# Kernel tuning notes

Hardware: AMD Instinct MI355X
Metric: run time of the kernel (lower is better)

## Reference

```python
import jax, jax.numpy as jnp
import numpy as np

F = 32  # node channels (both convs)


def ecc_conv(x, src, dst, e, fgn_w, fgn_b, root, bias):
    """Edge-conditioned conv: per-edge kernel from edge feats, gather-matmul-scatter."""
    n_nodes = x.shape[0]
    n_edges = e.shape[0]
    f_in = x.shape[1]
    # filter-generating network: (E, S) -> (E, F_in*F_out) -> (E, F_in, F_out)
    kernels = (e @ fgn_w + fgn_b).reshape(n_edges, f_in, F)
    # gather source node feats, per-edge matmul
    messages = jnp.einsum('ef,efo->eo', x[src], kernels)
    # scatter-sum to target nodes
    agg = jax.ops.segment_sum(messages, dst, num_segments=n_nodes)
    return jax.nn.relu(agg + x @ root + bias)


def setup_inputs() -> dict:
    key = jax.random.key(0)
    ks = jax.random.split(key, 12)
    N, E, S = 50000, 200000, 16
    s = 0.05  # small init scale to keep activations bounded through relu
    return {
        'x': jax.random.normal(ks[0], (N, F), jnp.float32),
        'e': jax.random.normal(ks[1], (E, S), jnp.float32),
        'src': jax.random.randint(ks[2], (E,), 0, N, jnp.int32),
        'dst': jax.random.randint(ks[3], (E,), 0, N, jnp.int32),
        'fgn_w1': jax.random.normal(ks[4], (S, F * F), jnp.float32) * s,
        'fgn_b1': jnp.zeros((F * F,), jnp.float32),
        'root1': jax.random.normal(ks[5], (F, F), jnp.float32) * s,
        'bias1': jnp.zeros((F,), jnp.float32),
        'fgn_w2': jax.random.normal(ks[6], (S, F * F), jnp.float32) * s,
        'fgn_b2': jnp.zeros((F * F,), jnp.float32),
        'root2': jax.random.normal(ks[7], (F, F), jnp.float32) * s,
        'bias2': jnp.zeros((F,), jnp.float32),
        'dense_w': jax.random.normal(ks[8], (F, 1), jnp.float32) * s,
        'dense_b': jnp.zeros((1,), jnp.float32),
    }


def reference(x, e, src, dst, fgn_w1, fgn_b1, root1, bias1,
              fgn_w2, fgn_b2, root2, bias2, dense_w, dense_b):
    h = ecc_conv(x, src, dst, e, fgn_w1, fgn_b1, root1, bias1)
    h = ecc_conv(h, src, dst, e, fgn_w2, fgn_b2, root2, bias2)
    pooled = jnp.sum(h, axis=0)          # global sum pool over nodes -> (F,)
    return pooled @ dense_w + dense_b    # (1,)
```

## Files before the change

kernel.cpp:

```cpp
#include <hip/hip_runtime.h>
#include <hip/hip_bf16.h>

#define F 32
#define S 16

typedef short v8s __attribute__((ext_vector_type(8)));
typedef float v4f __attribute__((ext_vector_type(4)));

__device__ __forceinline__ float bf_lo(unsigned u) { return __uint_as_float(u << 16); }
__device__ __forceinline__ float bf_hi(unsigned u) { return __uint_as_float(u & 0xffff0000u); }
__device__ __forceinline__ unsigned short f2bf(float f) {
    __hip_bfloat16 h = __float2bfloat16(f);
    return *(unsigned short*)&h;
}
__device__ __forceinline__ unsigned pack2(float a, float b) {
    __hip_bfloat162 h2 = __float22bfloat162_rn(make_float2(a, b));
    return *(unsigned*)&h2;
}
static inline size_t align256(size_t b) { return (b + 255) & ~(size_t)255; }

__global__ __launch_bounds__(256) void convert_w2(
    const float* __restrict__ w1, const float* __restrict__ b1, const float* __restrict__ r1,
    const float* __restrict__ w2, const float* __restrict__ b2, const float* __restrict__ r2,
    unsigned short* __restrict__ Wf1, unsigned short* __restrict__ Wf2,
    unsigned short* __restrict__ Rt1, unsigned short* __restrict__ Rt2)
{
    const int PER = 34 * 512 + 32 * 32;
    int tid = blockIdx.x * blockDim.x + threadIdx.x;
    if (tid >= 2 * PER) return;
    const int layer = tid / PER;
    const int rem   = tid % PER;
    const float* w = layer ? w2 : w1;
    const float* b = layer ? b2 : b1;
    const float* r = layer ? r2 : r1;
    if (rem < 34 * 512) {
        const int fi   = rem >> 9;
        const int rr   = rem & 511;
        const int lane = rr >> 3;
        const int j    = rr & 7;
        const int half = fi & 1;
        const int ck   = fi >> 1;
        const int o    = (half << 4) | (lane & 15);
        const int k    = ck * 32 + (lane >> 4) * 8 + j;
        const int s    = k >> 5, f = k & 31;
        const float v  = (s < S) ? w[s * (F * F) + f * F + o] : b[f * F + o];
        (layer ? Wf2 : Wf1)[rem] = f2bf(v);
    } else {
        const int q = rem - 34 * 512;
        const int o = q >> 5, f = q & 31;
        (layer ? Rt2 : Rt1)[o * F + f] = f2bf(r[f * F + o]);
    }
}

__global__ __launch_bounds__(256) void hist_kernel(
    const int* __restrict__ dst, int* __restrict__ cnt, int E)
{
    int e = blockIdx.x * blockDim.x + threadIdx.x;
    if (e < E) atomicAdd(&cnt[dst[e]], 1);
}

__global__ __launch_bounds__(256) void scan_partial(
    const int* __restrict__ cnt, int* __restrict__ partial, int N)
{
    const int i = blockIdx.x * 256 + threadIdx.x;
    int v = (i < N) ? cnt[i] : 0;
    #pragma unroll
    for (int off = 32; off > 0; off >>= 1) v += __shfl_down(v, off, 64);
    __shared__ int wsum[4];
    const int wave = threadIdx.x >> 6, lane = threadIdx.x & 63;
    if (lane == 0) wsum[wave] = v;
    __syncthreads();
    if (threadIdx.x == 0)
        partial[blockIdx.x] = wsum[0] + wsum[1] + wsum[2] + wsum[3];
}

__global__ void scan_top(int* __restrict__ partial, int M)
{
    const int t = threadIdx.x;
    int carry = 0;
    for (int base = 0; base < M; base += 64) {
        const int i = base + t;
        const int v0 = (i < M) ? partial[i] : 0;
        int v = v0;
        #pragma unroll
        for (int off = 1; off < 64; off <<= 1) {
            int u = __shfl_up(v, off, 64);
            if (t >= off) v += u;
        }
        if (i < M) partial[i] = carry + (v - v0);
        carry += __shfl(v, 63, 64);
    }
}

__global__ __launch_bounds__(256) void scan_final(
    const int* __restrict__ cnt, const int* __restrict__ partial,
    int* __restrict__ cursor, int* __restrict__ rowptr, int N)
{
    const int i = blockIdx.x * 256 + threadIdx.x;
    const int v0 = (i < N) ? cnt[i] : 0;
    int v = v0;
    const int wave = threadIdx.x >> 6, lane = threadIdx.x & 63;
    #pragma unroll
    for (int off = 1; off < 64; off <<= 1) {
        int u = __shfl_up(v, off, 64);
        if (lane >= off) v += u;
    }
    __shared__ int wsum[4];
    if (lane == 63) wsum[wave] = v;
    __syncthreads();
    int woff = 0;
    for (int ww = 0; ww < 4; ++ww) woff += (ww < wave) ? wsum[ww] : 0;
    if (i < N) {
        const int excl = partial[blockIdx.x] + woff + (v - v0);
        cursor[i] = excl;
        rowptr[i] = excl;
    }
}

__global__ __launch_bounds__(256) void scatter_kernel(
    const int* __restrict__ dst, int* __restrict__ cursor,
    int* __restrict__ perm, int E)
{
    int e = blockIdx.x * blockDim.x + threadIdx.x;
    if (e < E) {
        int p = atomicAdd(&cursor[dst[e]], 1);
        perm[p] = e;
    }
}

__global__ __launch_bounds__(256) void esort_kernel(
    const float* __restrict__ ef, const int* __restrict__ src,
    const int* __restrict__ perm,
    float* __restrict__ ef_s, int* __restrict__ src_s, int E)
{
    const int gid = blockIdx.x * blockDim.x + threadIdx.x;
    const int slot = gid >> 2;
    if (slot >= E) return;
    const int q = gid & 3;
    const int e = perm[slot];
    ((float4*)(ef_s + (size_t)slot * S))[q] = ((const float4*)(ef + (size_t)e * S))[q];
    if (q == 0) src_s[slot] = src[e];
}

__global__ __launch_bounds__(256) void edge_msg(
    const float* __restrict__ xin,
    const float* __restrict__ ef_s,
    const int* __restrict__ src_s,
    const unsigned short* __restrict__ Wf,
    unsigned short* __restrict__ msg,
    int E)
{
    __shared__ v8s Wl[34 * 64];
    const int tid  = threadIdx.x;
    const int w    = tid >> 6;
    const int lane = tid & 63;
    const int lid  = lane & 15;
    const int quad = lane >> 4;

    {
        const uint4* s = (const uint4*)Wf;
        uint4* d = (uint4*)Wl;
        #pragma unroll
        for (int i = 0; i < 9; ++i) {
            const int idx = tid + 256 * i;
            if (idx < 2176) d[idx] = s[idx];
        }
    }
    __syncthreads();

    const int nTiles = (E + 15) >> 4;
    const int stride = gridDim.x * 4;
    int tile = blockIdx.x * 4 + w;
    if (tile >= nTiles) return;

    int  slot = tile * 16 + lid;
    bool live = (slot < E);
    int  s0   = live ? slot : 0;
    int  sn   = src_s[s0];
    const float4* xp = (const float4*)(xin + (size_t)sn * F + quad * 8);
    float4 xv0 = xp[0], xv1 = xp[1];
    const float4* efv = (const float4*)(ef_s + (size_t)s0 * S);
    float4 c0 = efv[0], c1 = efv[1], c2 = efv[2], c3 = efv[3];

    while (true) {
        const int nextTile = tile + stride;
        float4 nxv0, nxv1, nc0, nc1, nc2, nc3;
        bool nlive = false;
        if (nextTile < nTiles) {
            const int  ns_  = nextTile * 16 + lid;
            nlive = (ns_ < E);
            const int  ns0_ = nlive ? ns_ : 0;
            const int  nsn  = src_s[ns0_];
            const float4* nxp = (const float4*)(xin + (size_t)nsn * F + quad * 8);
            nxv0 = nxp[0]; nxv1 = nxp[1];
            const float4* nefv = (const float4*)(ef_s + (size_t)ns0_ * S);
            nc0 = nefv[0]; nc1 = nefv[1]; nc2 = nefv[2]; nc3 = nefv[3];
        }

        const float cs[S] = {c0.x, c0.y, c0.z, c0.w, c1.x, c1.y, c1.z, c1.w,
                             c2.x, c2.y, c2.z, c2.w, c3.x, c3.y, c3.z, c3.w};

        v4f acc0 = {0.f, 0.f, 0.f, 0.f};
        v4f acc1 = {0.f, 0.f, 0.f, 0.f};

        #pragma unroll
        for (int ck = 0; ck < S; ++ck) {
            const float sc = cs[ck];
            union { v8s s8; uint4 u4; } fr;
            fr.u4.x = pack2(sc * xv0.x, sc * xv0.y);
            fr.u4.y = pack2(sc * xv0.z, sc * xv0.w);
            fr.u4.z = pack2(sc * xv1.x, sc * xv1.y);
            fr.u4.w = pack2(sc * xv1.z, sc * xv1.w);
            acc0 = __builtin_amdgcn_mfma_f32_16x16x32_bf16(Wl[(2 * ck) * 64 + lane],     fr.s8, acc0, 0, 0, 0);
            acc1 = __builtin_amdgcn_mfma_f32_16x16x32_bf16(Wl[(2 * ck + 1) * 64 + lane], fr.s8, acc1, 0, 0, 0);
        }
        {
            union { v8s s8; uint4 u4; } fr;
            fr.u4.x = pack2(xv0.x, xv0.y);
            fr.u4.y = pack2(xv0.z, xv0.w);
            fr.u4.z = pack2(xv1.x, xv1.y);
            fr.u4.w = pack2(xv1.z, xv1.w);
            acc0 = __builtin_amdgcn_mfma_f32_16x16x32_bf16(Wl[32 * 64 + lane], fr.s8, acc0, 0, 0, 0);
            acc1 = __builtin_amdgcn_mfma_f32_16x16x32_bf16(Wl[33 * 64 + lane], fr.s8, acc1, 0, 0, 0);
        }

        if (live) {
            unsigned short* mp = msg + (size_t)slot * 32;
            uint2 p0, p1;
            p0.x = pack2(acc0[0], acc0[1]);
            p0.y = pack2(acc0[2], acc0[3]);
            p1.x = pack2(acc1[0], acc1[1]);
            p1.y = pack2(acc1[2], acc1[3]);
            *(uint2*)(mp + quad * 4)      = p0;
            *(uint2*)(mp + 16 + quad * 4) = p1;
        }

        if (nextTile >= nTiles) break;
        tile = nextTile;
        slot = tile * 16 + lid;
        live = nlive;
        xv0 = nxv0; xv1 = nxv1;
        c0 = nc0; c1 = nc1; c2 = nc2; c3 = nc3;
    }
}

__global__ __launch_bounds__(256) void rootsum(
    const float* __restrict__ in,
    const unsigned short* __restrict__ msg,
    const int* __restrict__ rowptr,
    const int* __restrict__ cnt,
    const unsigned short* __restrict__ Rt,
    const float* __restrict__ bias,
    float* __restrict__ h,
    int N)
{
    __shared__ float acc[64 * 33];
    __shared__ unsigned short As[64 * F];
    const int tid  = threadIdx.x;
    const int n0   = blockIdx.x * 64;
    const int w    = tid >> 6;
    const int lane = tid & 63;
    const int lid  = lane & 15;
    const int quad = lane >> 4;

    {
        const int nl = tid >> 2;
        const int kq = tid & 3;
        int n = n0 + nl; if (n > N - 1) n = N - 1;
        const float4* xp = (const float4*)(in + (size_t)n * F + kq * 8);
        float4 v0 = xp[0], v1 = xp[1];
        uint4 pk;
        pk.x = pack2(v0.x, v0.y);
        pk.y = pack2(v0.z, v0.w);
        pk.z = pack2(v1.x, v1.y);
        pk.w = pack2(v1.z, v1.w);
        const int slot = ((nl >> 4) * 4 + kq) * 16 + (nl & 15);
        *(uint4*)(As + slot * 8) = pk;
    }

    {
        const int nl = tid >> 2;
        const int oq = tid & 3;
        const int n  = n0 + nl;
        float a[8];
        #pragma unroll
        for (int j = 0; j < 8; ++j) a[j] = 0.f;
        if (n < N) {
            const int k0 = rowptr[n];
            const int k1 = k0 + cnt[n];
            for (int k = k0; k < k1; ++k) {
                const uint4 q = *(const uint4*)(msg + (size_t)k * 32 + oq * 8);
                a[0] += bf_lo(q.x); a[1] += bf_hi(q.x);
                a[2] += bf_lo(q.y); a[3] += bf_hi(q.y);
                a[4] += bf_lo(q.z); a[5] += bf_hi(q.z);
                a[6] += bf_lo(q.w); a[7] += bf_hi(q.w);
            }
        }
        float* ap = acc + nl * 33 + oq * 8;
        #pragma unroll
        for (int j = 0; j < 8; ++j) ap[j] = a[j];
    }
    __syncthreads();

    const int jt  = w & 1;
    const int ns0 = (w >> 1) * 2;
    const v8s rf = *(const v8s*)(Rt + (size_t)(jt * 16 + lid) * F + quad * 8);
    const int o0 = jt * 16 + quad * 4;
    const float4 bs = *(const float4*)(bias + o0);

    #pragma unroll
    for (int i = 0; i < 2; ++i) {
        const int ns = ns0 + i;
        const v8s af = *(const v8s*)(As + (((ns * 4 + quad) * 16) + lid) * 8);
        v4f d = {0.f, 0.f, 0.f, 0.f};
        d = __builtin_amdgcn_mfma_f32_16x16x32_bf16(rf, af, d, 0, 0, 0);
        const int n = n0 + ns * 16 + lid;
        if (n < N) {
            const float* ap = acc + (ns * 16 + lid) * 33 + o0;
            float4 hv;
            hv.x = fmaxf(d[0] + ap[0] + bs.x, 0.f);
            hv.y = fmaxf(d[1] + ap[1] + bs.y, 0.f);
            hv.z = fmaxf(d[2] + ap[2] + bs.z, 0.f);
            hv.w = fmaxf(d[3] + ap[3] + bs.w, 0.f);
            *(float4*)(h + (size_t)n * F + o0) = hv;
        }
    }
}

__global__ __launch_bounds__(256) void pool_kernel(
    const float* __restrict__ h, float* __restrict__ pooled, int N)
{
    const int c = threadIdx.x & (F - 1);
    float p = 0.0f;
    for (int n = blockIdx.x * 8 + (threadIdx.x >> 5); n < N; n += gridDim.x * 8)
        p += h[(size_t)n * F + c];
    __shared__ float red[256];
    red[threadIdx.x] = p;
    __syncthreads();
    for (int off = 128; off >= F; off >>= 1) {
        if (threadIdx.x < off) red[threadIdx.x] += red[threadIdx.x + off];
        __syncthreads();
    }
    if (threadIdx.x < F) atomicAdd(&pooled[threadIdx.x], red[threadIdx.x]);
}

__global__ void final_kernel(
    const float* __restrict__ pooled, const float* __restrict__ dw,
    const float* __restrict__ db, float* __restrict__ out)
{
    const int o = threadIdx.x;
    float v = (o < F) ? pooled[o] * dw[o] : 0.0f;
    #pragma unroll
    for (int off = 32; off > 0; off >>= 1) v += __shfl_down(v, off, 64);
    if (o == 0) out[0] = v + db[0];
}

__global__ __launch_bounds__(256, 2) void ecc_edge_slow(
    const float* __restrict__ x, const float* __restrict__ ef,
    const int* __restrict__ src, const int* __restrict__ dst,
    const float* __restrict__ W, const float* __restrict__ B,
    float* __restrict__ agg, int E)
{
    const int tid = blockIdx.x * blockDim.x + threadIdx.x;
    const bool live = (tid < E);
    const int e = live ? tid : (E - 1);
    const int sn = src[e], dn = dst[e];
    float xr[F];
    const float4* xp = (const float4*)(x + (size_t)sn * F);
    #pragma unroll
    for (int i = 0; i < F / 4; ++i) {
        float4 v = xp[i];
        xr[4*i+0] = v.x; xr[4*i+1] = v.y; xr[4*i+2] = v.z; xr[4*i+3] = v.w;
    }
    float acc[F];
    #pragma unroll
    for (int o = 0; o < F; ++o) acc[o] = 0.0f;
    const float* erow = ef + (size_t)e * S;
    for (int s = 0; s < S; ++s) {
        const float es = erow[s];
        const float* Ws = W + s * (F * F);
        #pragma unroll
        for (int f = 0; f < F; ++f) {
            const float z = es * xr[f];
            #pragma unroll
            for (int o = 0; o < F; ++o) acc[o] = fmaf(z, Ws[f * F + o], acc[o]);
        }
    }
    #pragma unroll
    for (int f = 0; f < F; ++f) {
        const float xf = xr[f];
        #pragma unroll
        for (int o = 0; o < F; ++o) acc[o] = fmaf(xf, B[f * F + o], acc[o]);
    }
    if (live) {
        float* ap = agg + (size_t)dn * F;
        #pragma unroll
        for (int o = 0; o < F; ++o) atomicAdd(ap + o, acc[o]);
    }
}

__global__ __launch_bounds__(256) void ecc_node_slow(
    const float* __restrict__ xin, const float* __restrict__ root,
    const float* __restrict__ bias, float* __restrict__ h, int N)
{
    int t = blockIdx.x * blockDim.x + threadIdx.x;
    if (t >= N * F) return;
    const int n = t >> 5, o = t & (F - 1);
    const float* xrow = xin + (size_t)n * F;
    float v = h[t] + bias[o];
    #pragma unroll
    for (int f = 0; f < F; ++f) v = fmaf(xrow[f], root[f * F + o], v);
    h[t] = fmaxf(v, 0.0f);
}

extern "C" void kernel_launch(void* const* d_in, const int* in_sizes, int n_in,
                              void* d_out, int out_size, void* d_ws, size_t ws_size,
                              hipStream_t stream) {
    const float* x      = (const float*)d_in[0];
    const float* efeat  = (const float*)d_in[1];
    const int*   src    = (const int*)d_in[2];
    const int*   dst    = (const int*)d_in[3];
    const float* fgn_w1 = (const float*)d_in[4];
    const float* fgn_b1 = (const float*)d_in[5];
    const float* root1  = (const float*)d_in[6];
    const float* bias1  = (const float*)d_in[7];
    const float* fgn_w2 = (const float*)d_in[8];
    const float* fgn_b2 = (const float*)d_in[9];
    const float* root2  = (const float*)d_in[10];
    const float* bias2  = (const float*)d_in[11];
    const float* dense_w = (const float*)d_in[12];
    const float* dense_b = (const float*)d_in[13];

    const int N = in_sizes[0] / F;
    const int E = in_sizes[2];

    const int gridP = (N + 255) / 256;

    const size_t pooledB = 256;
    const size_t cntB    = align256((size_t)N * 4);
    const size_t rowB    = align256((size_t)N * 4);
    const size_t curB    = align256((size_t)N * 4);
    const size_t partB   = align256((size_t)gridP * 4);
    const size_t permB   = align256((size_t)E * 4);
    const size_t efsB    = align256((size_t)E * S * 4);
    const size_t srcsB   = align256((size_t)E * 4);
    const size_t msgB    = align256((size_t)E * 32 * 2);
    const size_t hB      = (size_t)N * F * 4;
    const size_t wfB     = align256((size_t)34 * 512 * 2);
    const size_t rtB     = align256((size_t)32 * 32 * 2);

    const size_t offCnt  = pooledB;
    const size_t offRow  = offCnt + cntB;
    const size_t offCur  = offRow + rowB;
    const size_t offPart = offCur + curB;
    const size_t offPerm = offPart + partB;
    const size_t offEfs  = offPerm + permB;
    const size_t offSrcs = offEfs + efsB;
    const size_t offMsg  = offSrcs + srcsB;
    const size_t offH1   = offMsg + msgB;
    const size_t offH2   = offH1 + hB;
    const size_t offW1   = offH2 + hB;
    const size_t offW2   = offW1 + wfB;
    const size_t offR1   = offW2 + wfB;
    const size_t offR2   = offR1 + rtB;
    const size_t need    = offR2 + rtB;

    const int eB         = (E + 255) / 256;
    const int nodeBlocks = (N * F + 255) / 256;

    if (ws_size >= need) {
        float* pooled = (float*)d_ws;
        int* cnt     = (int*)((char*)d_ws + offCnt);
        int* rowptr  = (int*)((char*)d_ws + offRow);
        int* cursor  = (int*)((char*)d_ws + offCur);
        int* partial = (int*)((char*)d_ws + offPart);
        int* perm    = (int*)((char*)d_ws + offPerm);
        float* ef_s  = (float*)((char*)d_ws + offEfs);
        int*   src_s = (int*)((char*)d_ws + offSrcs);
        unsigned short* msg = (unsigned short*)((char*)d_ws + offMsg);
        float* h1    = (float*)((char*)d_ws + offH1);
        float* h2    = (float*)((char*)d_ws + offH2);
        unsigned short* Wf1 = (unsigned short*)((char*)d_ws + offW1);
        unsigned short* Wf2 = (unsigned short*)((char*)d_ws + offW2);
        unsigned short* Rt1 = (unsigned short*)((char*)d_ws + offR1);
        unsigned short* Rt2 = (unsigned short*)((char*)d_ws + offR2);

        hipMemsetAsync(d_ws, 0, pooledB + cntB, stream);

        convert_w2<<<(2 * 18432 + 255) / 256, 256, 0, stream>>>(
            fgn_w1, fgn_b1, root1, fgn_w2, fgn_b2, root2, Wf1, Wf2, Rt1, Rt2);

        hist_kernel   <<<eB, 256, 0, stream>>>(dst, cnt, E);
        scan_partial  <<<gridP, 256, 0, stream>>>(cnt, partial, N);
        scan_top      <<<1, 64, 0, stream>>>(partial, gridP);
        scan_final    <<<gridP, 256, 0, stream>>>(cnt, partial, cursor, rowptr, N);
        scatter_kernel<<<eB, 256, 0, stream>>>(dst, cursor, perm, E);
        esort_kernel  <<<(E * 4 + 255) / 256, 256, 0, stream>>>(efeat, src, perm, ef_s, src_s, E);

        const int nTiles     = (E + 15) / 16;
        int edgeBlocks = (nTiles + 3) / 4;
        if (edgeBlocks > 1024) edgeBlocks = 1024;
        const int rsBlocks   = (N + 63) / 64;

        edge_msg<<<edgeBlocks, 256, 0, stream>>>(x, ef_s, src_s, Wf1, msg, E);
        rootsum <<<rsBlocks, 256, 0, stream>>>(x, msg, rowptr, cnt, Rt1, bias1, h1, N);

        edge_msg<<<edgeBlocks, 256, 0, stream>>>(h1, ef_s, src_s, Wf2, msg, E);
        rootsum <<<rsBlocks, 256, 0, stream>>>(h1, msg, rowptr, cnt, Rt2, bias2, h2, N);

        pool_kernel <<<512, 256, 0, stream>>>(h2, pooled, N);
        final_kernel<<<1, 64, 0, stream>>>(pooled, dense_w, dense_b, (float*)d_out);
    } else {
        float* agg1   = (float*)d_ws;
        float* agg2   = agg1 + (size_t)N * F;
        float* pooled = agg2 + (size_t)N * F;
        hipMemsetAsync(d_ws, 0, (2 * (size_t)N * F + F) * sizeof(float), stream);
        ecc_edge_slow<<<eB, 256, 0, stream>>>(x, efeat, src, dst, fgn_w1, fgn_b1, agg1, E);
        ecc_node_slow<<<nodeBlocks, 256, 0, stream>>>(x, root1, bias1, agg1, N);
        ecc_edge_slow<<<eB, 256, 0, stream>>>(agg1, efeat, src, dst, fgn_w2, fgn_b2, agg2, E);
        ecc_node_slow<<<nodeBlocks, 256, 0, stream>>>(agg1, root2, bias2, agg2, N);
        pool_kernel <<<512, 256, 0, stream>>>(agg2, pooled, N);
        final_kernel<<<1, 64, 0, stream>>>(pooled, dense_w, dense_b, (float*)d_out);
    }
}
```

Baseline: 196.7 us.

## Fuse prep kernels, scatter with edge sort, and pooling into second rootsum

```diff
diff --git a/kernel.cpp b/kernel.cpp
--- a/kernel.cpp
+++ b/kernel.cpp
@@ -19,44 +19,43 @@
 }
 static inline size_t align256(size_t b) { return (b + 255) & ~(size_t)255; }
 
-__global__ __launch_bounds__(256) void convert_w2(
+__global__ __launch_bounds__(256) void prep_kernel(
     const float* __restrict__ w1, const float* __restrict__ b1, const float* __restrict__ r1,
     const float* __restrict__ w2, const float* __restrict__ b2, const float* __restrict__ r2,
     unsigned short* __restrict__ Wf1, unsigned short* __restrict__ Wf2,
-    unsigned short* __restrict__ Rt1, unsigned short* __restrict__ Rt2)
+    unsigned short* __restrict__ Rt1, unsigned short* __restrict__ Rt2,
+    const int* __restrict__ dst, int* __restrict__ cnt, int E)
 {
     const int PER = 34 * 512 + 32 * 32;
-    int tid = blockIdx.x * blockDim.x + threadIdx.x;
-    if (tid >= 2 * PER) return;
-    const int layer = tid / PER;
-    const int rem   = tid % PER;
-    const float* w = layer ? w2 : w1;
-    const float* b = layer ? b2 : b1;
-    const float* r = layer ? r2 : r1;
-    if (rem < 34 * 512) {
-        const int fi   = rem >> 9;
-        const int rr   = rem & 511;
-        const int lane = rr >> 3;
-        const int j    = rr & 7;
-        const int half = fi & 1;
-        const int ck   = fi >> 1;
-        const int o    = (half << 4) | (lane & 15);
-        const int k    = ck * 32 + (lane >> 4) * 8 + j;
-        const int s    = k >> 5, f = k & 31;
-        const float v  = (s < S) ? w[s * (F * F) + f * F + o] : b[f * F + o];
-        (layer ? Wf2 : Wf1)[rem] = f2bf(v);
+    if (blockIdx.x < 144) {
+        int tid = blockIdx.x * blockDim.x + threadIdx.x;
+        if (tid >= 2 * PER) return;
+        const int layer = tid / PER;
+        const int rem   = tid % PER;
+        const float* w = layer ? w2 : w1;
+        const float* b = layer ? b2 : b1;
+        const float* r = layer ? r2 : r1;
+        if (rem < 34 * 512) {
+            const int fi   = rem >> 9;
+            const int rr   = rem & 511;
+            const int lane = rr >> 3;
+            const int j    = rr & 7;
+            const int half = fi & 1;
+            const int ck   = fi >> 1;
+            const int o    = (half << 4) | (lane & 15);
+            const int k    = ck * 32 + (lane >> 4) * 8 + j;
+            const int s    = k >> 5, f = k & 31;
+            const float v  = (s < S) ? w[s * (F * F) + f * F + o] : b[f * F + o];
+            (layer ? Wf2 : Wf1)[rem] = f2bf(v);
+        } else {
+            const int q = rem - 34 * 512;
+            const int o = q >> 5, f = q & 31;
+            (layer ? Rt2 : Rt1)[o * F + f] = f2bf(r[f * F + o]);
+        }
     } else {
-        const int q = rem - 34 * 512;
-        const int o = q >> 5, f = q & 31;
-        (layer ? Rt2 : Rt1)[o * F + f] = f2bf(r[f * F + o]);
-    }
-}
-
-__global__ __launch_bounds__(256) void hist_kernel(
-    const int* __restrict__ dst, int* __restrict__ cnt, int E)
-{
-    int e = blockIdx.x * blockDim.x + threadIdx.x;
-    if (e < E) atomicAdd(&cnt[dst[e]], 1);
+        const int e = (blockIdx.x - 144) * blockDim.x + threadIdx.x;
+        if (e < E) atomicAdd(&cnt[dst[e]], 1);
+    }
 }
 
 __global__ __launch_bounds__(256) void scan_partial(
@@ -117,29 +116,19 @@
     }
 }
 
-__global__ __launch_bounds__(256) void scatter_kernel(
-    const int* __restrict__ dst, int* __restrict__ cursor,
-    int* __restrict__ perm, int E)
-{
-    int e = blockIdx.x * blockDim.x + threadIdx.x;
-    if (e < E) {
-        int p = atomicAdd(&cursor[dst[e]], 1);
-        perm[p] = e;
-    }
-}
-
-__global__ __launch_bounds__(256) void esort_kernel(
-    const float* __restrict__ ef, const int* __restrict__ src,
-    const int* __restrict__ perm,
+__global__ __launch_bounds__(256) void scatter_fused(
+    const int* __restrict__ dst, const int* __restrict__ src,
+    const float* __restrict__ ef, int* __restrict__ cursor,
     float* __restrict__ ef_s, int* __restrict__ src_s, int E)
 {
-    const int gid = blockIdx.x * blockDim.x + threadIdx.x;
-    const int slot = gid >> 2;
-    if (slot >= E) return;
-    const int q = gid & 3;
-    const int e = perm[slot];
-    ((float4*)(ef_s + (size_t)slot * S))[q] = ((const float4*)(ef + (size_t)e * S))[q];
-    if (q == 0) src_s[slot] = src[e];
+    const int e = blockIdx.x * blockDim.x + threadIdx.x;
+    if (e >= E) return;
+    const int p = atomicAdd(&cursor[dst[e]], 1);
+    src_s[p] = src[e];
+    const float4* s = (const float4*)(ef + (size_t)e * S);
+    float4 a = s[0], b = s[1], c = s[2], d = s[3];
+    float4* o = (float4*)(ef_s + (size_t)p * S);
+    o[0] = a; o[1] = b; o[2] = c; o[3] = d;
 }
 
 __global__ __launch_bounds__(256) void edge_msg(
@@ -177,21 +166,22 @@
     bool live = (slot < E);
     int  s0   = live ? slot : 0;
     int  sn   = src_s[s0];
-    const float4* xp = (const float4*)(xin + (size_t)sn * F + quad * 8);
-    float4 xv0 = xp[0], xv1 = xp[1];
+    const v4f* xp = (const v4f*)(xin + (size_t)sn * F + quad * 8);
+    v4f xv0 = xp[0], xv1 = xp[1];
     const float4* efv = (const float4*)(ef_s + (size_t)s0 * S);
     float4 c0 = efv[0], c1 = efv[1], c2 = efv[2], c3 = efv[3];
 
     while (true) {
         const int nextTile = tile + stride;
-        float4 nxv0, nxv1, nc0, nc1, nc2, nc3;
+        v4f nxv0, nxv1;
+        float4 nc0, nc1, nc2, nc3;
         bool nlive = false;
         if (nextTile < nTiles) {
             const int  ns_  = nextTile * 16 + lid;
             nlive = (ns_ < E);
             const int  ns0_ = nlive ? ns_ : 0;
             const int  nsn  = src_s[ns0_];
-            const float4* nxp = (const float4*)(xin + (size_t)nsn * F + quad * 8);
+            const v4f* nxp = (const v4f*)(xin + (size_t)nsn * F + quad * 8);
             nxv0 = nxp[0]; nxv1 = nxp[1];
             const float4* nefv = (const float4*)(ef_s + (size_t)ns0_ * S);
             nc0 = nefv[0]; nc1 = nefv[1]; nc2 = nefv[2]; nc3 = nefv[3];
@@ -206,20 +196,22 @@
         #pragma unroll
         for (int ck = 0; ck < S; ++ck) {
             const float sc = cs[ck];
+            const v4f a0 = xv0 * sc;
+            const v4f a1 = xv1 * sc;
             union { v8s s8; uint4 u4; } fr;
-            fr.u4.x = pack2(sc * xv0.x, sc * xv0.y);
-            fr.u4.y = pack2(sc * xv0.z, sc * xv0.w);
-            fr.u4.z = pack2(sc * xv1.x, sc * xv1.y);
-            fr.u4.w = pack2(sc * xv1.z, sc * xv1.w);
+            fr.u4.x = pack2(a0[0], a0[1]);
+            fr.u4.y = pack2(a0[2], a0[3]);
+            fr.u4.z = pack2(a1[0], a1[1]);
+            fr.u4.w = pack2(a1[2], a1[3]);
             acc0 = __builtin_amdgcn_mfma_f32_16x16x32_bf16(Wl[(2 * ck) * 64 + lane],     fr.s8, acc0, 0, 0, 0);
             acc1 = __builtin_amdgcn_mfma_f32_16x16x32_bf16(Wl[(2 * ck + 1) * 64 + lane], fr.s8, acc1, 0, 0, 0);
         }
         {
             union { v8s s8; uint4 u4; } fr;
-            fr.u4.x = pack2(xv0.x, xv0.y);
-            fr.u4.y = pack2(xv0.z, xv0.w);
-            fr.u4.z = pack2(xv1.x, xv1.y);
-            fr.u4.w = pack2(xv1.z, xv1.w);
+            fr.u4.x = pack2(xv0[0], xv0[1]);
+            fr.u4.y = pack2(xv0[2], xv0[3]);
+            fr.u4.z = pack2(xv1[0], xv1[1]);
+            fr.u4.w = pack2(xv1[2], xv1[3]);
             acc0 = __builtin_amdgcn_mfma_f32_16x16x32_bf16(Wl[32 * 64 + lane], fr.s8, acc0, 0, 0, 0);
             acc1 = __builtin_amdgcn_mfma_f32_16x16x32_bf16(Wl[33 * 64 + lane], fr.s8, acc1, 0, 0, 0);
         }
@@ -252,10 +244,12 @@
     const unsigned short* __restrict__ Rt,
     const float* __restrict__ bias,
     float* __restrict__ h,
+    float* __restrict__ bs,
     int N)
 {
     __shared__ float acc[64 * 33];
     __shared__ unsigned short As[64 * F];
+    __shared__ float poolbuf[4][16];
     const int tid  = threadIdx.x;
     const int n0   = blockIdx.x * 64;
     const int w    = tid >> 6;
@@ -306,7 +300,9 @@
     const int ns0 = (w >> 1) * 2;
     const v8s rf = *(const v8s*)(Rt + (size_t)(jt * 16 + lid) * F + quad * 8);
     const int o0 = jt * 16 + quad * 4;
-    const float4 bs = *(const float4*)(bias + o0);
+    const float4 bs4 = *(const float4*)(bias + o0);
+
+    float psum[4] = {0.f, 0.f, 0.f, 0.f};
 
     #pragma unroll
     for (int i = 0; i < 2; ++i) {
@@ -315,15 +311,60 @@
         v4f d = {0.f, 0.f, 0.f, 0.f};
         d = __builtin_amdgcn_mfma_f32_16x16x32_bf16(rf, af, d, 0, 0, 0);
         const int n = n0 + ns * 16 + lid;
+        const float* ap = acc + (ns * 16 + lid) * 33 + o0;
+        float4 hv;
+        hv.x = fmaxf(d[0] + ap[0] + bs4.x, 0.f);
+        hv.y = fmaxf(d[1] + ap[1] + bs4.y, 0.f);
+        hv.z = fmaxf(d[2] + ap[2] + bs4.z, 0.f);
+        hv.w = fmaxf(d[3] + ap[3] + bs4.w, 0.f);
         if (n < N) {
-            const float* ap = acc + (ns * 16 + lid) * 33 + o0;
-            float4 hv;
-            hv.x = fmaxf(d[0] + ap[0] + bs.x, 0.f);
-            hv.y = fmaxf(d[1] + ap[1] + bs.y, 0.f);
-            hv.z = fmaxf(d[2] + ap[2] + bs.z, 0.f);
-            hv.w = fmaxf(d[3] + ap[3] + bs.w, 0.f);
-            *(float4*)(h + (size_t)n * F + o0) = hv;
-        }
+            if (h) *(float4*)(h + (size_t)n * F + o0) = hv;
+            psum[0] += hv.x; psum[1] += hv.y; psum[2] += hv.z; psum[3] += hv.w;
+        }
+    }
+
+    if (bs) {
+        #pragma unroll
+        for (int m = 1; m < 16; m <<= 1) {
+            psum[0] += __shfl_xor(psum[0], m, 64);
+            psum[1] += __shfl_xor(psum[1], m, 64);
+            psum[2] += __shfl_xor(psum[2], m, 64);
+            psum[3] += __shfl_xor(psum[3], m, 64);
+        }
+        if (lid == 0) {
+            #pragma unroll
+            for (int j = 0; j < 4; ++j) poolbuf[w][quad * 4 + j] = psum[j];
+        }
+        __syncthreads();
+        if (tid < 32) {
+            const int jt2 = tid >> 4, idx = tid & 15;
+            bs[(size_t)blockIdx.x * 32 + tid] = poolbuf[jt2][idx] + poolbuf[jt2 + 2][idx];
+        }
+    }
+}
+
+__global__ __launch_bounds__(256) void final_fused(
+    const float* __restrict__ bs, int nb,
+    const float* __restrict__ dw, const float* __restrict__ db,
+    float* __restrict__ out)
+{
+    const int ch = threadIdx.x & 31, g = threadIdx.x >> 5;
+    float s = 0.f;
+    for (int b = g; b < nb; b += 8) s += bs[(size_t)b * 32 + ch];
+    __shared__ float red[256];
+    red[threadIdx.x] = s;
+    __syncthreads();
+    if (threadIdx.x < 128) red[threadIdx.x] += red[threadIdx.x + 128];
+    __syncthreads();
+    if (threadIdx.x < 64) red[threadIdx.x] += red[threadIdx.x + 64];
+    __syncthreads();
+    if (threadIdx.x < 32) red[threadIdx.x] = (red[threadIdx.x] + red[threadIdx.x + 32]) * dw[threadIdx.x];
+    __syncthreads();
+    if (threadIdx.x == 0) {
+        float t = 0.f;
+        #pragma unroll
+        for (int i = 0; i < 32; ++i) t += red[i];
+        out[0] = t + db[0];
     }
 }
 
@@ -434,18 +475,19 @@
     const int N = in_sizes[0] / F;
     const int E = in_sizes[2];
 
-    const int gridP = (N + 255) / 256;
+    const int gridP    = (N + 255) / 256;
+    const int rsBlocks = (N + 63) / 64;
 
     const size_t pooledB = 256;
     const size_t cntB    = align256((size_t)N * 4);
     const size_t rowB    = align256((size_t)N * 4);
     const size_t curB    = align256((size_t)N * 4);
     const size_t partB   = align256((size_t)gridP * 4);
-    const size_t permB   = align256((size_t)E * 4);
     const size_t efsB    = align256((size_t)E * S * 4);
     const size_t srcsB   = align256((size_t)E * 4);
     const size_t msgB    = align256((size_t)E * 32 * 2);
     const size_t hB      = (size_t)N * F * 4;
+    const size_t bsB     = align256((size_t)rsBlocks * 32 * 4);
     const size_t wfB     = align256((size_t)34 * 512 * 2);
     const size_t rtB     = align256((size_t)32 * 32 * 2);
 
@@ -453,13 +495,12 @@
     const size_t offRow  = offCnt + cntB;
     const size_t offCur  = offRow + rowB;
     const size_t offPart = offCur + curB;
-    const size_t offPerm = offPart + partB;
-    const size_t offEfs  = offPerm + permB;
+    const size_t offEfs  = offPart + partB;
     const size_t offSrcs = offEfs + efsB;
     const size_t offMsg  = offSrcs + srcsB;
     const size_t offH1   = offMsg + msgB;
-    const size_t offH2   = offH1 + hB;
-    const size_t offW1   = offH2 + hB;
+    const size_t offBs   = offH1 + hB;
+    const size_t offW1   = offBs + bsB;
     const size_t offW2   = offW1 + wfB;
     const size_t offR1   = offW2 + wfB;
     const size_t offR2   = offR1 + rtB;
@@ -469,17 +510,15 @@
     const int nodeBlocks = (N * F + 255) / 256;
 
     if (ws_size >= need) {
-        float* pooled = (float*)d_ws;
         int* cnt     = (int*)((char*)d_ws + offCnt);
         int* rowptr  = (int*)((char*)d_ws + offRow);
         int* cursor  = (int*)((char*)d_ws + offCur);
         int* partial = (int*)((char*)d_ws + offPart);
-        int* perm    = (int*)((char*)d_ws + offPerm);
         float* ef_s  = (float*)((char*)d_ws + offEfs);
         int*   src_s = (int*)((char*)d_ws + offSrcs);
         unsigned short* msg = (unsigned short*)((char*)d_ws + offMsg);
         float* h1    = (float*)((char*)d_ws + offH1);
-        float* h2    = (float*)((char*)d_ws + offH2);
+        float* bsum  = (float*)((char*)d_ws + offBs);
         unsigned short* Wf1 = (unsigned short*)((char*)d_ws + offW1);
         unsigned short* Wf2 = (unsigned short*)((char*)d_ws + offW2);
         unsigned short* Rt1 = (unsigned short*)((char*)d_ws + offR1);
@@ -487,29 +526,26 @@
 
         hipMemsetAsync(d_ws, 0, pooledB + cntB, stream);
 
-        convert_w2<<<(2 * 18432 + 255) / 256, 256, 0, stream>>>(
-            fgn_w1, fgn_b1, root1, fgn_w2, fgn_b2, root2, Wf1, Wf2, Rt1, Rt2);
-
-        hist_kernel   <<<eB, 256, 0, stream>>>(dst, cnt, E);
-        scan_partial  <<<gridP, 256, 0, stream>>>(cnt, partial, N);
-        scan_top      <<<1, 64, 0, stream>>>(partial, gridP);
-        scan_final    <<<gridP, 256, 0, stream>>>(cnt, partial, cursor, rowptr, N);
-        scatter_kernel<<<eB, 256, 0, stream>>>(dst, cursor, perm, E);
-        esort_kernel  <<<(E * 4 + 255) / 256, 256, 0, stream>>>(efeat, src, perm, ef_s, src_s, E);
-
-        const int nTiles     = (E + 15) / 16;
+        prep_kernel<<<144 + eB, 256, 0, stream>>>(
+            fgn_w1, fgn_b1, root1, fgn_w2, fgn_b2, root2,
+            Wf1, Wf2, Rt1, Rt2, dst, cnt, E);
+
+        scan_partial <<<gridP, 256, 0, stream>>>(cnt, partial, N);
+        scan_top     <<<1, 64, 0, stream>>>(partial, gridP);
+        scan_final   <<<gridP, 256, 0, stream>>>(cnt, partial, cursor, rowptr, N);
+        scatter_fused<<<eB, 256, 0, stream>>>(dst, src, efeat, cursor, ef_s, src_s, E);
+
+        const int nTiles = (E + 15) / 16;
         int edgeBlocks = (nTiles + 3) / 4;
         if (edgeBlocks > 1024) edgeBlocks = 1024;
-        const int rsBlocks   = (N + 63) / 64;
 
         edge_msg<<<edgeBlocks, 256, 0, stream>>>(x, ef_s, src_s, Wf1, msg, E);
-        rootsum <<<rsBlocks, 256, 0, stream>>>(x, msg, rowptr, cnt, Rt1, bias1, h1, N);
+        rootsum <<<rsBlocks, 256, 0, stream>>>(x, msg, rowptr, cnt, Rt1, bias1, h1, nullptr, N);
 
         edge_msg<<<edgeBlocks, 256, 0, stream>>>(h1, ef_s, src_s, Wf2, msg, E);
-        rootsum <<<rsBlocks, 256, 0, stream>>>(h1, msg, rowptr, cnt, Rt2, bias2, h2, N);
-
-        pool_kernel <<<512, 256, 0, stream>>>(h2, pooled, N);
-        final_kernel<<<1, 64, 0, stream>>>(pooled, dense_w, dense_b, (float*)d_out);
+        rootsum <<<rsBlocks, 256, 0, stream>>>(h1, msg, rowptr, cnt, Rt2, bias2, nullptr, bsum, N);
+
+        final_fused<<<1, 256, 0, stream>>>(bsum, rsBlocks, dense_w, dense_b, (float*)d_out);
     } else {
         float* agg1   = (float*)d_ws;
         float* agg2   = agg1 + (size_t)N * F;
```

Result: slower. 207.5 us (+5.5%).
